# Kernel tuning notes

Hardware: AMD Instinct MI355X
Metric: run time of the kernel (lower is better)

## Reference

```python
import jax, jax.numpy as jnp
import numpy as np

M = 4          # num_models
B = 128        # per-model batch
C = 10         # num_classes
K = 32         # num_centroids
F = 512        # feature_dimension
NZ = 512       # noise_dimension
H = 512        # hidden_dimension
SIGMA = 1.0    # length_scale (not learnable)


def be_fc(x, W, r, s, b=None):
    # BatchEnsemble (Ensemble_orderFC): x is [M*N, in], rows ordered by model.
    N = x.shape[0] // M
    xm = x.reshape(M, N, -1) * r[:, None, :]
    out = jnp.einsum('mni,io->mno', xm, W) * s[:, None, :]
    if b is not None:
        out = out + b[:, None, :]
    return out.reshape(M * N, -1)


def setup_inputs() -> dict:
    key = jax.random.key(0)
    ks = jax.random.split(key, 16)
    sc = lambda fan_in: 1.0 / np.sqrt(fan_in)
    inp = {
        'x': jax.random.normal(ks[0], (M * B, F), dtype=jnp.float32),
        'proto_noise': jax.random.normal(ks[1], (C * K, NZ), dtype=jnp.float32),
        # layer_W: F -> F*C, bias=False
        'W_lw': jax.random.normal(ks[2], (F, F * C), dtype=jnp.float32) * sc(F),
        'r_lw': 1.0 + 0.1 * jax.random.normal(ks[3], (M, F), dtype=jnp.float32),
        's_lw': 1.0 + 0.1 * jax.random.normal(ks[4], (M, F * C), dtype=jnp.float32),
        # fc1_p: (C + NZ) -> H
        'W1': jax.random.normal(ks[5], (C + NZ, H), dtype=jnp.float32) * sc(C + NZ),
        'r1': 1.0 + 0.1 * jax.random.normal(ks[6], (M, C + NZ), dtype=jnp.float32),
        's1': 1.0 + 0.1 * jax.random.normal(ks[7], (M, H), dtype=jnp.float32),
        'b1': jnp.zeros((M, H), dtype=jnp.float32),
        # fc2_p: H -> F
        'W2': jax.random.normal(ks[8], (H, F), dtype=jnp.float32) * sc(H),
        'r2': 1.0 + 0.1 * jax.random.normal(ks[9], (M, H), dtype=jnp.float32),
        's2': 1.0 + 0.1 * jax.random.normal(ks[10], (M, F), dtype=jnp.float32),
        'b2': jnp.zeros((M, F), dtype=jnp.float32),
    }
    return inp


def reference(x, proto_noise, W_lw, r_lw, s_lw, W1, r1, s1, b1, W2, r2, s2, b2):
    # ---- get_prototype ----
    onehot = jnp.repeat(jnp.eye(C, dtype=x.dtype), K, axis=0)        # [C*K, C]
    proto_in = jnp.concatenate([proto_noise, onehot], axis=1)        # [C*K, NZ+C]
    proto_in = jnp.tile(proto_in, (M, 1))                            # [M*C*K, NZ+C]
    h = jax.nn.relu(be_fc(proto_in, W1, r1, s1, b1))
    proto = be_fc(h, W2, r2, s2, b2).reshape(M, C, K, F)

    # ---- last_layer ----
    z = be_fc(x, W_lw, r_lw, s_lw)                                   # [M*B, F*C]
    z = z.reshape(M * B, F, C)

    # ---- output_layer: broadcast RBF squared-distance reduction ----
    zt = jnp.transpose(z.reshape(M, B, F, C), (0, 1, 3, 2))          # [M, B, C, F]
    diff = zt[:, :, :, None, :] - proto[:, None, :, :, :]            # [M, B, C, K, F]
    distances = -(diff ** 2).mean(axis=(-1, -2)) / (2.0 * SIGMA ** 2)  # [M, B, C]

    logit = distances.reshape(-1, C)                                 # [M*B, C]
    return jnp.exp(logit)
```

## Files before the change

kernel.cpp:

```cpp
#include <hip/hip_runtime.h>
#include <math.h>

#define MM 4
#define BB 128
#define CC 10
#define KK 32
#define FF 512
#define HH 512
#define NP 320
#define OUTW 5120

using bf16x8 = __attribute__((ext_vector_type(8))) short;
using f32x4  = __attribute__((ext_vector_type(4))) float;

__device__ __forceinline__ unsigned short f2bf(float f) {
    unsigned int u = __float_as_uint(f);
    u += 0x7FFFu + ((u >> 16) & 1u);
    return (unsigned short)(u >> 16);
}

template<int EPI, int ASRC, int BSRC, int WR, int WC, int I, int J,
         int KSTEPS, int KREALB, int RPM, int NCOLS>
__device__ __forceinline__ void gemm_tile(
    const int bx, const int by,
    const unsigned short* __restrict__ Abf, const float* __restrict__ Af32,
    const float* __restrict__ ascale,
    const unsigned short* __restrict__ Btbf, const float* __restrict__ Bf32,
    const float* __restrict__ s, const float* __restrict__ bias,
    const float* __restrict__ auxr, void* __restrict__ outv,
    float* __restrict__ auxw, unsigned short* smem)
{
    constexpr int TR = WR * I * 16;
    constexpr int TC = WC * J * 16;
    constexpr int BUFE = (TR + TC) * 32;
    const int t = threadIdx.x;
    const int lane = t & 63;
    const int w = t >> 6;
    const int wr = w / WC, wc = w % WC;
    const int l15 = lane & 15, l4 = lane >> 4;
    const int rowT = by * TR, colT = bx * TC;
    const int m = rowT / RPM;

    constexpr bool AGUARD = (TR * 4 < 256);
    const bool aact = !AGUARD || (t < TR * 4);
    const int asrow = t >> 2, ag = t & 3;
    const int stA = asrow * 32 + ((ag ^ ((asrow >> 1) & 3)) * 8);
    const unsigned short* gA = nullptr;
    const float* gAf = nullptr;
    const float* scp = nullptr;
    int cn = 0;
    if constexpr (ASRC == 0) {
        if (aact) gA = Abf + (size_t)(rowT + asrow) * 512 + ag * 8;
    } else {
        gAf = Af32 + (size_t)((rowT % NP) + asrow) * 512 + ag * 8;
        scp = ascale + (size_t)m * 522 + ag * 8;
        cn = ((rowT % NP) + asrow) >> 5;
    }
    const int bsrow = t >> 2, bg = t & 3;
    const int stB0 = bsrow * 32 + ((bg ^ ((bsrow >> 1) & 3)) * 8);
    const int bcol = t & 63, bkg = t >> 6;
    const int stB1 = bcol * 32 + ((bkg ^ ((bcol >> 1) & 3)) * 8);
    const unsigned short* gB = nullptr;
    if constexpr (BSRC == 0)
        gB = Btbf + (size_t)(colT + bsrow) * 512 + bg * 8;

    int offA[I], offB[J];
#pragma unroll
    for (int i = 0; i < I; ++i) {
        int rA = wr * (I * 16) + i * 16 + l15;
        offA[i] = rA * 32 + ((l4 ^ ((rA >> 1) & 3)) * 8);
    }
#pragma unroll
    for (int j = 0; j < J; ++j) {
        int rB = wc * (J * 16) + j * 16 + l15;
        offB[j] = rB * 32 + ((l4 ^ ((rB >> 1) & 3)) * 8);
    }

    f32x4 acc[I][J];
#pragma unroll
    for (int i = 0; i < I; ++i)
#pragma unroll
        for (int j = 0; j < J; ++j) acc[i][j] = (f32x4){0.f, 0.f, 0.f, 0.f};

    uint4 ra, rb;
    float4 nf0, nf1, ns0, ns1;
    float rbf[8];

#define FETCH(KS)                                                              \
    {                                                                          \
        const int k0 = (KS) * 32;                                              \
        if constexpr (ASRC == 0) {                                             \
            if (aact) ra = *(const uint4*)(gA + k0);                           \
        } else {                                                               \
            if (k0 < 512) {                                                    \
                nf0 = *(const float4*)(gAf + k0);                              \
                nf1 = *(const float4*)(gAf + k0 + 4);                          \
                ns0 = *(const float4*)(scp + k0);                              \
                ns1 = *(const float4*)(scp + k0 + 4);                          \
            }                                                                  \
        }                                                                      \
        if constexpr (BSRC == 0) {                                             \
            rb = *(const uint4*)(gB + k0);                                     \
        } else {                                                               \
            _Pragma("unroll")                                                  \
            for (int q = 0; q < 8; ++q) {                                      \
                int gk = k0 + bkg * 8 + q;                                     \
                rbf[q] = (gk < KREALB)                                         \
                    ? Bf32[(size_t)gk * NCOLS + colT + bcol] : 0.f;            \
            }                                                                  \
        }                                                                      \
    }

#define WRITE(KS, BUF)                                                         \
    {                                                                          \
        const int k0 = (KS) * 32;                                              \
        unsigned short* As_ = smem + (BUF) * BUFE;                             \
        unsigned short* Bs_ = As_ + TR * 32;                                   \
        if constexpr (ASRC == 0) {                                             \
            if (aact) *(uint4*)(As_ + stA) = ra;                               \
        } else {                                                               \
            union { unsigned short u[8]; uint4 q; } o;                         \
            if (k0 < 512) {                                                    \
                float vv[8] = {nf0.x, nf0.y, nf0.z, nf0.w,                     \
                               nf1.x, nf1.y, nf1.z, nf1.w};                    \
                float ss[8] = {ns0.x, ns0.y, ns0.z, ns0.w,                     \
                               ns1.x, ns1.y, ns1.z, ns1.w};                    \
                _Pragma("unroll")                                              \
                for (int q = 0; q < 8; ++q) o.u[q] = f2bf(vv[q] * ss[q]);      \
            } else {                                                           \
                _Pragma("unroll")                                              \
                for (int q = 0; q < 8; ++q) {                                  \
                    int gk = k0 + ag * 8 + q;                                  \
                    float v = (gk < 522 && (gk - 512) == cn)                   \
                        ? ascale[(size_t)m * 522 + gk] : 0.f;                  \
                    o.u[q] = f2bf(v);                                          \
                }                                                              \
            }                                                                  \
            *(uint4*)(As_ + stA) = o.q;                                        \
        }                                                                      \
        if constexpr (BSRC == 0) {                                             \
            *(uint4*)(Bs_ + stB0) = rb;                                        \
        } else {                                                               \
            union { unsigned short u[8]; uint4 q; } o;                         \
            _Pragma("unroll")                                                  \
            for (int q = 0; q < 8; ++q) o.u[q] = f2bf(rbf[q]);                 \
            *(uint4*)(Bs_ + stB1) = o.q;                                       \
        }                                                                      \
    }

    FETCH(0);
    WRITE(0, 0);
    __syncthreads();

#pragma unroll 1
    for (int ks = 0; ks < KSTEPS; ++ks) {
        const int cur = ks & 1;
        if (ks + 1 < KSTEPS) FETCH(ks + 1);
        const unsigned short* As_ = smem + cur * BUFE;
        const unsigned short* Bs_ = As_ + TR * 32;
        bf16x8 af[I], bfv[J];
#pragma unroll
        for (int i = 0; i < I; ++i) af[i] = *(const bf16x8*)(As_ + offA[i]);
#pragma unroll
        for (int j = 0; j < J; ++j) bfv[j] = *(const bf16x8*)(Bs_ + offB[j]);
#pragma unroll
        for (int i = 0; i < I; ++i)
#pragma unroll
            for (int j = 0; j < J; ++j)
                acc[i][j] = __builtin_amdgcn_mfma_f32_16x16x32_bf16(
                    af[i], bfv[j], acc[i][j], 0, 0, 0);
        if (ks + 1 < KSTEPS) {
            WRITE(ks + 1, cur ^ 1);
            __syncthreads();
        }
    }
#undef FETCH
#undef WRITE

    if constexpr (EPI == 0) {
#pragma unroll
        for (int j = 0; j < J; ++j) {
            const int col = colT + wc * (J * 16) + j * 16 + l15;
            const float sv = s[(size_t)m * NCOLS + col];
            const float bv = bias[(size_t)m * NCOLS + col];
            const float rv = auxr[(size_t)m * NCOLS + col];
#pragma unroll
            for (int i = 0; i < I; ++i)
#pragma unroll
                for (int ir = 0; ir < 4; ++ir) {
                    const int row = rowT + wr * (I * 16) + i * 16 + l4 * 4 + ir;
                    float v = fmaxf(acc[i][j][ir] * sv + bv, 0.f) * rv;
                    ((unsigned short*)outv)[(size_t)row * NCOLS + col] = f2bf(v);
                }
        }
    } else if constexpr (EPI == 1) {
        static_assert(WR == 1 && I == 2 && J == 1, "EPI1 geometry");
        const int mq = rowT / NP;
        const int c = (rowT % NP) / KK;
        const int mc = mq * CC + c;
        const int col = colT + wc * 16 + l15;
        const float sv = s[(size_t)mq * NCOLS + col];
        const float bv = bias[(size_t)mq * NCOLS + col];
        float cs = 0.f, sq = 0.f;
#pragma unroll
        for (int i = 0; i < I; ++i)
#pragma unroll
            for (int ir = 0; ir < 4; ++ir) {
                float v = acc[i][0][ir] * sv + bv;
                cs += v;
                sq += v * v;
            }
        cs += __shfl_xor(cs, 16, 64);
        cs += __shfl_xor(cs, 32, 64);
        if (l4 == 0) ((float*)outv)[(size_t)mc * FF + col] = cs;
#pragma unroll
        for (int off = 1; off < 64; off <<= 1) sq += __shfl_xor(sq, off, 64);
        if (lane == 0) auxw[mc * 32 + bx * 4 + w] = sq;
    } else {
        static_assert(WR == 2 && WC == 2 && I == 2 && J == 2, "EPI2 geometry");
        const int cb = colT >> 9;
        const int slot = ((bx & 7) << 1) | wc;
        float sv[J], pv[J];
#pragma unroll
        for (int j = 0; j < J; ++j) {
            const int col = colT + wc * (J * 16) + j * 16 + l15;
            sv[j] = s[(size_t)m * NCOLS + (col & 511) * 10 + (col >> 9)];
            pv[j] = bias[(size_t)m * NCOLS + col];
        }
        float* dst = (float*)outv;
#pragma unroll
        for (int i = 0; i < I; ++i)
#pragma unroll
            for (int ir = 0; ir < 4; ++ir) {
                const int row = rowT + wr * (I * 16) + i * 16 + l4 * 4 + ir;
                float znv = 0.f, crv = 0.f;
#pragma unroll
                for (int j = 0; j < J; ++j) {
                    float v = acc[i][j][ir] * sv[j];
                    znv += v * v;
                    crv += v * pv[j];
                }
#pragma unroll
                for (int off = 1; off < 16; off <<= 1) {
                    znv += __shfl_xor(znv, off, 64);
                    crv += __shfl_xor(crv, off, 64);
                }
                if (l15 == 0) {
                    float2 o = {znv, crv};
                    *(float2*)(dst + ((size_t)(row * CC + cb) * 16 + slot) * 2) = o;
                }
            }
    }
}

__global__ __launch_bounds__(256) void k_phase1(
    const float* __restrict__ noise, const float* __restrict__ r1,
    const float* __restrict__ W1, const float* __restrict__ s1,
    const float* __restrict__ b1, const float* __restrict__ r2,
    const float* __restrict__ W_lw, const float* __restrict__ x,
    const float* __restrict__ r_lw,
    unsigned short* __restrict__ A2, unsigned short* __restrict__ Wlwt,
    unsigned short* __restrict__ xr)
{
    __shared__ __align__(16) unsigned short smem[8192];
    const int b = blockIdx.x;
    const int t = threadIdx.x;
    if (b < 160) {
        gemm_tile<0, 2, 1, 2, 2, 2, 2, 17, 522, NP, HH>(
            b % 8, b / 8, nullptr, noise, r1, nullptr, W1,
            s1, b1, r2, (void*)A2, nullptr, smem);
    } else if (b < 800) {
        unsigned short (*T)[65] = (unsigned short (*)[65])smem;
        const int bb = b - 160;
        const int n0 = (bb % 80) * 64, k0 = (bb / 80) * 64;
#pragma unroll
        for (int p = 0; p < 4; ++p) {
            int kk = (t >> 4) + p * 16;
            int nn = (t & 15) * 4;
            float4 v = *(const float4*)(W_lw + (size_t)(k0 + kk) * OUTW + n0 + nn);
            T[nn + 0][kk] = f2bf(v.x);
            T[nn + 1][kk] = f2bf(v.y);
            T[nn + 2][kk] = f2bf(v.z);
            T[nn + 3][kk] = f2bf(v.w);
        }
        __syncthreads();
#pragma unroll
        for (int p = 0; p < 2; ++p) {
            int n = (t >> 3) + p * 32;
            int kg = t & 7;
            union { unsigned short u[8]; uint4 v; } o;
#pragma unroll
            for (int q = 0; q < 8; ++q) o.u[q] = T[n][kg * 8 + q];
            int gn = n0 + n;
            int dr = (gn % 10) * 512 + gn / 10;
            *(uint4*)(Wlwt + (size_t)dr * 512 + k0 + kg * 8) = o.v;
        }
    } else {
        const int id = (b - 800) * 256 + t;
        const int row = id >> 6, g = id & 63;
        const int mq = row >> 7;
        const float* xp = x + (size_t)row * 512 + g * 8;
        const float* rp = r_lw + (size_t)mq * 512 + g * 8;
        union { unsigned short u[8]; uint4 v; } o;
#pragma unroll
        for (int q = 0; q < 8; ++q) o.u[q] = f2bf(xp[q] * rp[q]);
        *(uint4*)(xr + (size_t)row * 512 + g * 8) = o.v;
    }
}

__global__ __launch_bounds__(256) void k_phase2(
    const unsigned short* __restrict__ A2, const float* __restrict__ W2,
    const float* __restrict__ s2, const float* __restrict__ b2,
    float* __restrict__ psum, float* __restrict__ pn_part)
{
    __shared__ __align__(16) unsigned short smem[6144];
    gemm_tile<1, 0, 1, 1, 4, 2, 1, 16, 512, NP, FF>(
        blockIdx.x, blockIdx.y, A2, nullptr, nullptr, nullptr, W2,
        s2, b2, nullptr, (void*)psum, pn_part, smem);
}

__global__ __launch_bounds__(256) void k_phase3(
    const unsigned short* __restrict__ xr, const unsigned short* __restrict__ Wlwt,
    const float* __restrict__ s_lw, const float* __restrict__ psum,
    float* __restrict__ dist_part)
{
    __shared__ __align__(16) unsigned short smem[8192];
    gemm_tile<2, 0, 0, 2, 2, 2, 2, 16, 512, BB, OUTW>(
        blockIdx.x, blockIdx.y, xr, nullptr, nullptr, Wlwt, nullptr,
        s_lw, psum, nullptr, (void*)dist_part, nullptr, smem);
}

__global__ __launch_bounds__(256) void k_out(
    const float* __restrict__ dist_part, const float* __restrict__ pn_part,
    float* __restrict__ out)
{
    const int id = blockIdx.x * 256 + threadIdx.x;
    const int c = id % 10;
    const int mb = id / 10;
    const int mc = (mb >> 7) * 10 + c;
    const float* dp = dist_part + (size_t)id * 32;
    float zn = 0.f, cr = 0.f;
#pragma unroll
    for (int q = 0; q < 16; ++q) {
        zn += dp[q * 2];
        cr += dp[q * 2 + 1];
    }
    float pnv = 0.f;
#pragma unroll
    for (int q = 0; q < 32; ++q) pnv += pn_part[mc * 32 + q];
    const float inv = 1.f / (2.f * (float)KK * (float)FF);
    out[id] = expf(-((float)KK * zn - 2.f * cr + pnv) * inv);
}

extern "C" void kernel_launch(void* const* d_in, const int* in_sizes, int n_in,
                              void* d_out, int out_size, void* d_ws, size_t ws_size,
                              hipStream_t stream) {
    const float* x     = (const float*)d_in[0];
    const float* noise = (const float*)d_in[1];
    const float* W_lw  = (const float*)d_in[2];
    const float* r_lw  = (const float*)d_in[3];
    const float* s_lw  = (const float*)d_in[4];
    const float* W1    = (const float*)d_in[5];
    const float* r1    = (const float*)d_in[6];
    const float* s1    = (const float*)d_in[7];
    const float* b1    = (const float*)d_in[8];
    const float* W2    = (const float*)d_in[9];
    const float* r2    = (const float*)d_in[10];
    const float* s2    = (const float*)d_in[11];
    const float* b2    = (const float*)d_in[12];
    float* out = (float*)d_out;

    char* base = (char*)d_ws;
    float* psum          = (float*)(base + 0);
    float* pn_part       = (float*)(base + 81920);
    float* dist_part     = (float*)(base + 87040);
    unsigned short* A2   = (unsigned short*)(base + 742400);
    unsigned short* xr   = (unsigned short*)(base + 2053120);
    unsigned short* Wlwt = (unsigned short*)(base + 2577408);

    k_phase1<<<928, 256, 0, stream>>>(noise, r1, W1, s1, b1, r2, W_lw, x, r_lw,
                                      A2, Wlwt, xr);
    k_phase2<<<dim3(8, 40), 256, 0, stream>>>(A2, W2, s2, b2, psum, pn_part);
    k_phase3<<<dim3(80, 8), 256, 0, stream>>>(xr, Wlwt, s_lw, psum, dist_part);
    k_out<<<20, 256, 0, stream>>>(dist_part, pn_part, out);
}
```

Baseline: 56.16 us.

## Move W_lw transpose and x scaling into phase2 to overlap with W2 GEMM

Splits the first launch so it only runs the prototype fc1 GEMM tiles. The W_lw transpose/bf16 conversion and x*r_lw prep blocks are moved into the second launch, alongside the fc2 GEMM tiles, as a single flat grid. The intent is to rebalance work across the two dependent launches so the bandwidth-heavy transpose overlaps the small fc2 GEMM instead of lengthening phase1. The risk is that phase1 now launches only 160 blocks and underfills the GPU. Identifiers were also renamed and static_asserts added.

```diff
diff --git a/kernel.cpp b/kernel.cpp
--- a/kernel.cpp
+++ b/kernel.cpp
@@ -32,6 +32,7 @@
 {
     constexpr int TR = WR * I * 16;
     constexpr int TC = WC * J * 16;
+    static_assert(TR <= 64 && TC == 64, "staging geometry");
     constexpr int BUFE = (TR + TC) * 32;
     const int t = threadIdx.x;
     const int lane = t & 63;
@@ -52,6 +53,7 @@
     if constexpr (ASRC == 0) {
         if (aact) gA = Abf + (size_t)(rowT + asrow) * 512 + ag * 8;
     } else {
+        static_assert(TR == 64, "ASRC2 needs TR==64");
         gAf = Af32 + (size_t)((rowT % NP) + asrow) * 512 + ag * 8;
         scp = ascale + (size_t)m * 522 + ag * 8;
         cn = ((rowT % NP) + asrow) >> 5;
@@ -67,12 +69,12 @@
     int offA[I], offB[J];
 #pragma unroll
     for (int i = 0; i < I; ++i) {
-        int rA = wr * (I * 16) + i * 16 + l15;
+        const int rA = wr * (I * 16) + i * 16 + l15;
         offA[i] = rA * 32 + ((l4 ^ ((rA >> 1) & 3)) * 8);
     }
 #pragma unroll
     for (int j = 0; j < J; ++j) {
-        int rB = wc * (J * 16) + j * 16 + l15;
+        const int rB = wc * (J * 16) + j * 16 + l15;
         offB[j] = rB * 32 + ((l4 ^ ((rB >> 1) & 3)) * 8);
     }
 
@@ -88,23 +90,23 @@
 
 #define FETCH(KS)                                                              \
     {                                                                          \
-        const int k0 = (KS) * 32;                                              \
+        const int k0_ = (KS) * 32;                                             \
         if constexpr (ASRC == 0) {                                             \
-            if (aact) ra = *(const uint4*)(gA + k0);                           \
+            if (aact) ra = *(const uint4*)(gA + k0_);                          \
         } else {                                                               \
-            if (k0 < 512) {                                                    \
-                nf0 = *(const float4*)(gAf + k0);                              \
-                nf1 = *(const float4*)(gAf + k0 + 4);                          \
-                ns0 = *(const float4*)(scp + k0);                              \
-                ns1 = *(const float4*)(scp + k0 + 4);                          \
+            if (k0_ < 512) {                                                   \
+                nf0 = *(const float4*)(gAf + k0_);                             \
+                nf1 = *(const float4*)(gAf + k0_ + 4);                         \
+                ns0 = *(const float4*)(scp + k0_);                             \
+                ns1 = *(const float4*)(scp + k0_ + 4);                         \
             }                                                                  \
         }                                                                      \
         if constexpr (BSRC == 0) {                                             \
-            rb = *(const uint4*)(gB + k0);                                     \
+            rb = *(const uint4*)(gB + k0_);                                    \
         } else {                                                               \
             _Pragma("unroll")                                                  \
             for (int q = 0; q < 8; ++q) {                                      \
-                int gk = k0 + bkg * 8 + q;                                     \
+                const int gk = k0_ + bkg * 8 + q;                              \
                 rbf[q] = (gk < KREALB)                                         \
                     ? Bf32[(size_t)gk * NCOLS + colT + bcol] : 0.f;            \
             }                                                                  \
@@ -113,38 +115,38 @@
 
 #define WRITE(KS, BUF)                                                         \
     {                                                                          \
-        const int k0 = (KS) * 32;                                              \
+        const int k0_ = (KS) * 32;                                             \
         unsigned short* As_ = smem + (BUF) * BUFE;                             \
         unsigned short* Bs_ = As_ + TR * 32;                                   \
         if constexpr (ASRC == 0) {                                             \
             if (aact) *(uint4*)(As_ + stA) = ra;                               \
         } else {                                                               \
-            union { unsigned short u[8]; uint4 q; } o;                         \
-            if (k0 < 512) {                                                    \
+            union { unsigned short us[8]; uint4 q4; } o;                       \
+            if (k0_ < 512) {                                                   \
                 float vv[8] = {nf0.x, nf0.y, nf0.z, nf0.w,                     \
                                nf1.x, nf1.y, nf1.z, nf1.w};                    \
                 float ss[8] = {ns0.x, ns0.y, ns0.z, ns0.w,                     \
                                ns1.x, ns1.y, ns1.z, ns1.w};                    \
                 _Pragma("unroll")                                              \
-                for (int q = 0; q < 8; ++q) o.u[q] = f2bf(vv[q] * ss[q]);      \
+                for (int q = 0; q < 8; ++q) o.us[q] = f2bf(vv[q] * ss[q]);     \
             } else {                                                           \
                 _Pragma("unroll")                                              \
                 for (int q = 0; q < 8; ++q) {                                  \
-                    int gk = k0 + ag * 8 + q;                                  \
+                    const int gk = k0_ + ag * 8 + q;                           \
                     float v = (gk < 522 && (gk - 512) == cn)                   \
                         ? ascale[(size_t)m * 522 + gk] : 0.f;                  \
-                    o.u[q] = f2bf(v);                                          \
+                    o.us[q] = f2bf(v);                                         \
                 }                                                              \
             }                                                                  \
-            *(uint4*)(As_ + stA) = o.q;                                        \
+            *(uint4*)(As_ + stA) = o.q4;                                       \
         }                                                                      \
         if constexpr (BSRC == 0) {                                             \
             *(uint4*)(Bs_ + stB0) = rb;                                        \
         } else {                                                               \
-            union { unsigned short u[8]; uint4 q; } o;                         \
+            union { unsigned short us[8]; uint4 q4; } ob;                      \
             _Pragma("unroll")                                                  \
-            for (int q = 0; q < 8; ++q) o.u[q] = f2bf(rbf[q]);                 \
-            *(uint4*)(Bs_ + stB1) = o.q;                                       \
+            for (int q = 0; q < 8; ++q) ob.us[q] = f2bf(rbf[q]);               \
+            *(uint4*)(Bs_ + stB1) = ob.q4;                                     \
         }                                                                      \
     }
 
@@ -257,21 +259,32 @@
     const float* __restrict__ noise, const float* __restrict__ r1,
     const float* __restrict__ W1, const float* __restrict__ s1,
     const float* __restrict__ b1, const float* __restrict__ r2,
+    unsigned short* __restrict__ A2)
+{
+    __shared__ __align__(16) unsigned short smem[8192];
+    gemm_tile<0, 2, 1, 2, 2, 2, 2, 17, 522, NP, HH>(
+        blockIdx.x % 8, blockIdx.x / 8, nullptr, noise, r1, nullptr, W1,
+        s1, b1, r2, (void*)A2, nullptr, smem);
+}
+
+__global__ __launch_bounds__(256) void k_phase2(
+    const unsigned short* __restrict__ A2, const float* __restrict__ W2,
+    const float* __restrict__ s2, const float* __restrict__ b2,
     const float* __restrict__ W_lw, const float* __restrict__ x,
     const float* __restrict__ r_lw,
-    unsigned short* __restrict__ A2, unsigned short* __restrict__ Wlwt,
-    unsigned short* __restrict__ xr)
-{
-    __shared__ __align__(16) unsigned short smem[8192];
-    const int b = blockIdx.x;
+    float* __restrict__ psum, float* __restrict__ pn_part,
+    unsigned short* __restrict__ Wlwt, unsigned short* __restrict__ xr)
+{
+    __shared__ __align__(16) unsigned short smem[6144];
+    const int blk = blockIdx.x;
     const int t = threadIdx.x;
-    if (b < 160) {
-        gemm_tile<0, 2, 1, 2, 2, 2, 2, 17, 522, NP, HH>(
-            b % 8, b / 8, nullptr, noise, r1, nullptr, W1,
-            s1, b1, r2, (void*)A2, nullptr, smem);
-    } else if (b < 800) {
+    if (blk < 320) {
+        gemm_tile<1, 0, 1, 1, 4, 2, 1, 16, 512, NP, FF>(
+            blk % 8, blk / 8, A2, nullptr, nullptr, nullptr, W2,
+            s2, b2, nullptr, (void*)psum, pn_part, smem);
+    } else if (blk < 960) {
         unsigned short (*T)[65] = (unsigned short (*)[65])smem;
-        const int bb = b - 160;
+        const int bb = blk - 320;
         const int n0 = (bb % 80) * 64, k0 = (bb / 80) * 64;
 #pragma unroll
         for (int p = 0; p < 4; ++p) {
@@ -288,35 +301,24 @@
         for (int p = 0; p < 2; ++p) {
             int n = (t >> 3) + p * 32;
             int kg = t & 7;
-            union { unsigned short u[8]; uint4 v; } o;
-#pragma unroll
-            for (int q = 0; q < 8; ++q) o.u[q] = T[n][kg * 8 + q];
+            union { unsigned short us[8]; uint4 v; } o;
+#pragma unroll
+            for (int q = 0; q < 8; ++q) o.us[q] = T[n][kg * 8 + q];
             int gn = n0 + n;
             int dr = (gn % 10) * 512 + gn / 10;
             *(uint4*)(Wlwt + (size_t)dr * 512 + k0 + kg * 8) = o.v;
         }
     } else {
-        const int id = (b - 800) * 256 + t;
+        const int id = (blk - 960) * 256 + t;
         const int row = id >> 6, g = id & 63;
         const int mq = row >> 7;
         const float* xp = x + (size_t)row * 512 + g * 8;
         const float* rp = r_lw + (size_t)mq * 512 + g * 8;
-        union { unsigned short u[8]; uint4 v; } o;
-#pragma unroll
-        for (int q = 0; q < 8; ++q) o.u[q] = f2bf(xp[q] * rp[q]);
+        union { unsigned short us[8]; uint4 v; } o;
+#pragma unroll
+        for (int q = 0; q < 8; ++q) o.us[q] = f2bf(xp[q] * rp[q]);
         *(uint4*)(xr + (size_t)row * 512 + g * 8) = o.v;
     }
-}
-
-__global__ __launch_bounds__(256) void k_phase2(
-    const unsigned short* __restrict__ A2, const float* __restrict__ W2,
-    const float* __restrict__ s2, const float* __restrict__ b2,
-    float* __restrict__ psum, float* __restrict__ pn_part)
-{
-    __shared__ __align__(16) unsigned short smem[6144];
-    gemm_tile<1, 0, 1, 1, 4, 2, 1, 16, 512, NP, FF>(
-        blockIdx.x, blockIdx.y, A2, nullptr, nullptr, nullptr, W2,
-        s2, b2, nullptr, (void*)psum, pn_part, smem);
 }
 
 __global__ __launch_bounds__(256) void k_phase3(
@@ -378,9 +380,9 @@
     unsigned short* xr   = (unsigned short*)(base + 2053120);
     unsigned short* Wlwt = (unsigned short*)(base + 2577408);
 
-    k_phase1<<<928, 256, 0, stream>>>(noise, r1, W1, s1, b1, r2, W_lw, x, r_lw,
-                                      A2, Wlwt, xr);
-    k_phase2<<<dim3(8, 40), 256, 0, stream>>>(A2, W2, s2, b2, psum, pn_part);
+    k_phase1<<<160, 256, 0, stream>>>(noise, r1, W1, s1, b1, r2, A2);
+    k_phase2<<<1088, 256, 0, stream>>>(A2, W2, s2, b2, W_lw, x, r_lw,
+                                       psum, pn_part, Wlwt, xr);
     k_phase3<<<dim3(80, 8), 256, 0, stream>>>(xr, Wlwt, s_lw, psum, dist_part);
     k_out<<<20, 256, 0, stream>>>(dist_part, pn_part, out);
 }
```

After: 54.63 us. -2.7%, faster.
